# Performance work log

Measured on AMD Instinct MI355X. Metric: run time of the kernel, lower is better.

## Reference

```python
import jax, jax.numpy as jnp
import numpy as np

# Irreps config: 256x0e + 256x1e + 256x2e + 256x3e for both input and output.
MUL = 256
DIMS = (1, 3, 5, 7)          # (2l+1) for l = 0..3
OFFS = np.cumsum([0] + [MUL * d for d in DIMS]).tolist()  # [0,256,1024,2304,4096]
TOTAL_DIM = OFFS[-1]          # 4096
BATCH = 20000


def setup_inputs() -> dict:
    key = jax.random.key(0)
    ks = jax.random.split(key, 6)
    x = jax.random.normal(ks[0], (BATCH, TOTAL_DIM), dtype=jnp.float32)
    # per-path Linear weights, shape (mul_out, mul_in) like nn.Linear.weight,
    # kaiming_uniform_(a=sqrt(5)) => uniform(-1/sqrt(fan_in), 1/sqrt(fan_in))
    bound = 1.0 / np.sqrt(MUL)
    W = [jax.random.uniform(ks[i + 1], (MUL, MUL), dtype=jnp.float32,
                            minval=-bound, maxval=bound) for i in range(4)]
    bias = jnp.zeros((MUL,), dtype=jnp.float32)  # scalar (l=0) bias, init zeros
    return {"x": x, "W0": W[0], "W1": W[1], "W2": W[2], "W3": W[3], "bias": bias}


def reference(x, W0, W1, W2, W3, bias):
    Ws = (W0, W1, W2, W3)
    B = x.shape[0]
    out_chunks = []
    for l, (W, d) in enumerate(zip(Ws, DIMS)):
        # slice out this irrep block: (B, MUL*d) -> (B, MUL, d)
        xc = x[:, OFFS[l]:OFFS[l + 1]].reshape(B, MUL, d)
        # Linear over multiplicity channel: y[b,o,d] = sum_i W[o,i] * x[b,i,d]
        yc = jnp.einsum('oi,bid->bod', W, xc)
        out_chunks.append(yc.reshape(B, MUL * d))
    out = jnp.concatenate(out_chunks, axis=-1)  # (B, TOTAL_DIM)
    # bias on scalar (l=0) outputs only
    out = out.at[:, OFFS[0]:OFFS[1]].add(bias)
    return out
```

## Files before the change

### kernel.cpp

```cpp
#include <hip/hip_runtime.h>

#define BATCH_N 20000

typedef __attribute__((ext_vector_type(4))) float  f32x4;
typedef __attribute__((ext_vector_type(8))) __bf16 bf16x8;
typedef __attribute__((ext_vector_type(8))) short  s16x8;
typedef __attribute__((ext_vector_type(8))) unsigned short u16x8;
typedef __attribute__((ext_vector_type(4))) unsigned short u16x4;
typedef unsigned short u16;
typedef unsigned int   u32;

__device__ __forceinline__ u16 f2bf(float f) {
    union { float f; u32 u; } v; v.f = f;
    u32 r = v.u + 0x7fffu + ((v.u >> 16) & 1u);
    return (u16)(r >> 16);
}

template <typename C, typename V>
__device__ __forceinline__ auto mfma_bf16(V a, V b, C c, int)
    -> decltype(__builtin_amdgcn_mfma_f32_16x16x32_bf16(a, b, c, 0, 0, 0)) {
    return __builtin_amdgcn_mfma_f32_16x16x32_bf16(a, b, c, 0, 0, 0);
}
template <typename C, typename V>
__device__ __forceinline__ C mfma_bf16(V a, V b, C c, long) {
    return __builtin_amdgcn_mfma_f32_16x16x32_bf16(
        __builtin_bit_cast(s16x8, a), __builtin_bit_cast(s16x8, b), c, 0, 0, 0);
}

__device__ __forceinline__ bf16x8 cvt8(const float* p) {
    f32x4 v0 = *(const f32x4*)p;
    f32x4 v1 = *(const f32x4*)(p + 4);
    u16x8 raw = { f2bf(v0[0]), f2bf(v0[1]), f2bf(v0[2]), f2bf(v0[3]),
                  f2bf(v1[0]), f2bf(v1[1]), f2bf(v1[2]), f2bf(v1[3]) };
    return __builtin_bit_cast(bf16x8, raw);
}

template <typename WT>
__device__ __forceinline__ bf16x8 load_wfrag(const WT* p) {
    if constexpr (sizeof(WT) == 2) {
        return __builtin_bit_cast(bf16x8, *(const u16x8*)p);
    } else {
        return cvt8(p);
    }
}

template <typename WT>
__device__ __forceinline__ void run_l0(const float* __restrict__ x,
                                       const WT* __restrict__ W,
                                       const float* __restrict__ bias,
                                       float* __restrict__ out, int tile) {
    const int b0   = tile * 64;
    const int tid  = threadIdx.x;
    const int lane = tid & 63;
    const int wv   = tid >> 6;
    const int l15  = lane & 15;
    const int qd   = lane >> 4;

    f32x4 zero = {0.f, 0.f, 0.f, 0.f};
    f32x4 acc[4][4];
#pragma unroll
    for (int r = 0; r < 4; ++r)
#pragma unroll
        for (int c = 0; c < 4; ++c) acc[r][c] = zero;

    int brow[4];
#pragma unroll
    for (int r = 0; r < 4; ++r) {
        int b = b0 + r * 16 + l15;
        brow[r] = (b < BATCH_N) ? b : (BATCH_N - 1);
    }

#pragma unroll
    for (int kc = 0; kc < 4; ++kc) {
#pragma unroll
        for (int ks = 0; ks < 2; ++ks) {
            const int kg = kc * 64 + ks * 32 + qd * 8;
            bf16x8 a[4], bb[4];
#pragma unroll
            for (int r = 0; r < 4; ++r)
                a[r] = cvt8(x + (size_t)brow[r] * 4096 + kg);
#pragma unroll
            for (int c = 0; c < 4; ++c)
                bb[c] = load_wfrag(W + (size_t)(wv * 64 + c * 16 + l15) * 256 + kg);
#pragma unroll
            for (int r = 0; r < 4; ++r)
#pragma unroll
                for (int c = 0; c < 4; ++c)
                    acc[r][c] = mfma_bf16(a[r], bb[c], acc[r][c], 0);
        }
    }

    float bv[4];
#pragma unroll
    for (int c = 0; c < 4; ++c) bv[c] = bias[wv * 64 + c * 16 + l15];

#pragma unroll
    for (int r = 0; r < 4; ++r)
#pragma unroll
        for (int rg = 0; rg < 4; ++rg) {
            int b = b0 + r * 16 + qd * 4 + rg;
            if (b < BATCH_N) {
#pragma unroll
                for (int c = 0; c < 4; ++c)
                    out[(size_t)b * 4096 + wv * 64 + c * 16 + l15] = acc[r][c][rg] + bv[c];
            }
        }
}

template <int D, int NB, int OFF, typename WT>
__device__ __forceinline__ void run_gen(const float* __restrict__ x,
                                        const WT* __restrict__ W,
                                        float* __restrict__ out,
                                        u16* xs, int tile) {
    constexpr int CM = NB * D;
    const int b0   = tile * NB;
    const int nb   = (BATCH_N - b0 < NB) ? (BATCH_N - b0) : NB;
    const int cols = nb * D;
    const int tid  = threadIdx.x;
    const int lane = tid & 63;
    const int wv   = tid >> 6;
    const int l15  = lane & 15;
    const int qd   = lane >> 4;
    const int ob   = wv * 64;

    f32x4 zero = {0.f, 0.f, 0.f, 0.f};
    f32x4 acc[4][4];
#pragma unroll
    for (int r = 0; r < 4; ++r)
#pragma unroll
        for (int c = 0; c < 4; ++c) acc[r][c] = zero;

    for (int kc = 0; kc < 4; ++kc) {
#pragma unroll
        for (int g0 = 0; g0 < CM * 16; g0 += 256) {
            int g = g0 + tid;
            if (g < CM * 16) {
                int col = g % CM;
                int kq  = g / CM;
                if (col < cols) {
                    int bq = col / D;
                    int m  = col - bq * D;
                    const float* gp = x + (size_t)(b0 + bq) * 4096 + OFF +
                                      (kc * 64 + kq * 4) * D + m;
                    u16x4 u = { f2bf(gp[0]), f2bf(gp[D]), f2bf(gp[2 * D]), f2bf(gp[3 * D]) };
                    *(u16x4*)(xs + col * 72 + kq * 4) = u;
                }
            }
        }
        __syncthreads();

#pragma unroll
        for (int ks = 0; ks < 2; ++ks) {
            const int kg = kc * 64 + ks * 32 + qd * 8;
            const int kl = ks * 32 + qd * 8;
            bf16x8 a[4], bb[4];
#pragma unroll
            for (int r = 0; r < 4; ++r)
                a[r] = load_wfrag(W + (size_t)(ob + r * 16 + l15) * 256 + kg);
#pragma unroll
            for (int c = 0; c < 4; ++c)
                bb[c] = __builtin_bit_cast(bf16x8,
                            *(const u16x8*)(xs + (c * 16 + l15) * 72 + kl));
#pragma unroll
            for (int r = 0; r < 4; ++r)
#pragma unroll
                for (int c = 0; c < 4; ++c)
                    acc[r][c] = mfma_bf16(a[r], bb[c], acc[r][c], 0);
        }
        __syncthreads();
    }

#pragma unroll
    for (int c = 0; c < 4; ++c) {
        int col = c * 16 + l15;
        if (col < cols) {
            int bq = col / D;
            int m  = col - bq * D;
            float* op = out + (size_t)(b0 + bq) * 4096 + OFF + m;
#pragma unroll
            for (int r = 0; r < 4; ++r)
#pragma unroll
                for (int rg = 0; rg < 4; ++rg) {
                    int o = ob + r * 16 + qd * 4 + rg;
                    op[o * D] = acc[r][c][rg];
                }
        }
    }
}

template <typename WT>
__global__ __launch_bounds__(256) void so3_main(const float* __restrict__ x,
        const WT* __restrict__ W0, const WT* __restrict__ W1,
        const WT* __restrict__ W2, const WT* __restrict__ W3,
        const float* __restrict__ bias, float* __restrict__ out) {
    __shared__ __align__(16) u16 xs[64 * 72];
    int bid = blockIdx.x;
    if (bid < 313) {
        run_l0(x, W0, bias, out, bid);
    } else if (bid < 1266) {
        run_gen<3, 21, 256>(x, W1, out, xs, bid - 313);
    } else if (bid < 2933) {
        run_gen<5, 12, 1024>(x, W2, out, xs, bid - 1266);
    } else {
        run_gen<7, 9, 2304>(x, W3, out, xs, bid - 2933);
    }
}

__global__ __launch_bounds__(256) void w_to_bf16(const float* __restrict__ W0,
        const float* __restrict__ W1, const float* __restrict__ W2,
        const float* __restrict__ W3, u16* __restrict__ ws) {
    const float* Wt[4] = {W0, W1, W2, W3};
    const float* W = Wt[blockIdx.y];
    u16* o = ws + (size_t)blockIdx.y * 65536;
    int t = blockIdx.x * 256 + threadIdx.x;
    f32x4 v = ((const f32x4*)W)[t];
    u16x4 u = { f2bf(v[0]), f2bf(v[1]), f2bf(v[2]), f2bf(v[3]) };
    ((u16x4*)o)[t] = u;
}

extern "C" void kernel_launch(void* const* d_in, const int* in_sizes, int n_in,
                              void* d_out, int out_size, void* d_ws, size_t ws_size,
                              hipStream_t stream) {
    const float* x    = (const float*)d_in[0];
    const float* W0   = (const float*)d_in[1];
    const float* W1   = (const float*)d_in[2];
    const float* W2   = (const float*)d_in[3];
    const float* W3   = (const float*)d_in[4];
    const float* bias = (const float*)d_in[5];
    float* out = (float*)d_out;

    if (ws_size >= 4ull * 65536ull * sizeof(u16)) {
        u16* wsW = (u16*)d_ws;
        w_to_bf16<<<dim3(64, 4), 256, 0, stream>>>(W0, W1, W2, W3, wsW);
        so3_main<u16><<<5156, 256, 0, stream>>>(x, wsW, wsW + 65536,
                                                wsW + 2 * 65536, wsW + 3 * 65536,
                                                bias, out);
    } else {
        so3_main<float><<<5156, 256, 0, stream>>>(x, W0, W1, W2, W3, bias, out);
    }
}
```

Baseline: 725.5 us.

## Double-buffer x tiles in LDS with register prefetch across k-chunks

The l>0 path now stages x through registers. It loads and converts the next k-chunk from global memory while MFMAs run on the current LDS buffer, then writes it into a second LDS buffer. This drops one __syncthreads per iteration and hides global load latency behind compute. The cost is double the LDS footprint, extra staging registers, and a launch_bounds occupancy hint of 5 blocks per CU, which may force register spilling.

```diff
diff --git a/kernel.cpp b/kernel.cpp
--- a/kernel.cpp
+++ b/kernel.cpp
@@ -112,7 +112,10 @@
                                         const WT* __restrict__ W,
                                         float* __restrict__ out,
                                         u16* xs, int tile) {
-    constexpr int CM = NB * D;
+    constexpr int CM  = NB * D;
+    constexpr int NIT = CM * 16;
+    constexpr int SUB = (NIT + 255) / 256;
+    constexpr int BUF = 64 * 72;
     const int b0   = tile * NB;
     const int nb   = (BATCH_N - b0 < NB) ? (BATCH_N - b0) : NB;
     const int cols = nb * D;
@@ -130,24 +133,47 @@
 #pragma unroll
         for (int c = 0; c < 4; ++c) acc[r][c] = zero;
 
-    for (int kc = 0; kc < 4; ++kc) {
-#pragma unroll
-        for (int g0 = 0; g0 < CM * 16; g0 += 256) {
-            int g = g0 + tid;
-            if (g < CM * 16) {
-                int col = g % CM;
-                int kq  = g / CM;
+    u16x4 st[SUB];
+
+    auto gload = [&](int kc) {
+#pragma unroll
+        for (int s = 0; s < SUB; ++s) {
+            const int g = s * 256 + tid;
+            if (g < NIT) {
+                const int col = g % CM;
+                const int kq  = g / CM;
                 if (col < cols) {
-                    int bq = col / D;
-                    int m  = col - bq * D;
+                    const int bq = col / D;
+                    const int m  = col - bq * D;
                     const float* gp = x + (size_t)(b0 + bq) * 4096 + OFF +
                                       (kc * 64 + kq * 4) * D + m;
-                    u16x4 u = { f2bf(gp[0]), f2bf(gp[D]), f2bf(gp[2 * D]), f2bf(gp[3 * D]) };
-                    *(u16x4*)(xs + col * 72 + kq * 4) = u;
+                    st[s] = (u16x4){ f2bf(gp[0]), f2bf(gp[D]),
+                                     f2bf(gp[2 * D]), f2bf(gp[3 * D]) };
                 }
             }
         }
+    };
+    auto lwrite = [&](u16* buf) {
+#pragma unroll
+        for (int s = 0; s < SUB; ++s) {
+            const int g = s * 256 + tid;
+            if (g < NIT) {
+                const int col = g % CM;
+                const int kq  = g / CM;
+                if (col < cols)
+                    *(u16x4*)(buf + col * 72 + kq * 4) = st[s];
+            }
+        }
+    };
+
+    gload(0);
+    lwrite(xs);
+
+#pragma unroll
+    for (int kc = 0; kc < 4; ++kc) {
+        u16* cur = xs + (kc & 1) * BUF;
         __syncthreads();
+        if (kc < 3) gload(kc + 1);
 
 #pragma unroll
         for (int ks = 0; ks < 2; ++ks) {
@@ -160,14 +186,15 @@
 #pragma unroll
             for (int c = 0; c < 4; ++c)
                 bb[c] = __builtin_bit_cast(bf16x8,
-                            *(const u16x8*)(xs + (c * 16 + l15) * 72 + kl));
+                            *(const u16x8*)(cur + (c * 16 + l15) * 72 + kl));
 #pragma unroll
             for (int r = 0; r < 4; ++r)
 #pragma unroll
                 for (int c = 0; c < 4; ++c)
                     acc[r][c] = mfma_bf16(a[r], bb[c], acc[r][c], 0);
         }
-        __syncthreads();
+
+        if (kc < 3) lwrite(xs + ((kc + 1) & 1) * BUF);
     }
 
 #pragma unroll
@@ -189,11 +216,11 @@
 }
 
 template <typename WT>
-__global__ __launch_bounds__(256) void so3_main(const float* __restrict__ x,
+__global__ __launch_bounds__(256, 5) void so3_main(const float* __restrict__ x,
         const WT* __restrict__ W0, const WT* __restrict__ W1,
         const WT* __restrict__ W2, const WT* __restrict__ W3,
         const float* __restrict__ bias, float* __restrict__ out) {
-    __shared__ __align__(16) u16 xs[64 * 72];
+    __shared__ __align__(16) u16 xs[2 * 64 * 72];
     int bid = blockIdx.x;
     if (bid < 313) {
         run_l0(x, W0, bias, out, bid);
```

Measured after the change: 1.028 ms. 41.6% more time.

## Double-buffer LDS staging of x tiles with register prefetch in run_gen

Applied to the files above, without the earlier changes.

Converts the per-k-chunk global-to-LDS staging in the l>0 paths into a double-buffered software pipeline. The next chunk's global loads go into registers before the MFMAs and are written to the alternate LDS buffer afterwards, which removes one barrier per iteration and hides global load latency behind compute. Address computation is also hoisted out of the loop. This doubles LDS use per block and raises register pressure, which could lower occupancy.

```diff
diff --git a/kernel.cpp b/kernel.cpp
--- a/kernel.cpp
+++ b/kernel.cpp
@@ -112,7 +112,9 @@
                                         const WT* __restrict__ W,
                                         float* __restrict__ out,
                                         u16* xs, int tile) {
-    constexpr int CM = NB * D;
+    constexpr int CM  = NB * D;
+    constexpr int NIT = CM * 16;
+    constexpr int BUF = 64 * 72;
     const int b0   = tile * NB;
     const int nb   = (BATCH_N - b0 < NB) ? (BATCH_N - b0) : NB;
     const int cols = nb * D;
@@ -130,24 +132,43 @@
 #pragma unroll
         for (int c = 0; c < 4; ++c) acc[r][c] = zero;
 
+    const float* gp[4];
+    int          lo[4];
+    u16x4        st[4];
+#pragma unroll
+    for (int s = 0; s < 4; ++s) {
+        const int g   = s * 256 + tid;
+        const int col = g % CM;
+        const int kq  = g / CM;
+        const int bq  = col / D;
+        const int m   = col - bq * D;
+        const bool ok = (g < NIT) && (col < cols);
+        gp[s] = ok ? (x + (size_t)(b0 + bq) * 4096 + OFF + (kq * 4) * D + m)
+                   : x;
+        lo[s] = ok ? (col * 72 + kq * 4)
+                   : 64;
+    }
+
+#define GLOAD(kc_)                                                         \
+    _Pragma("unroll")                                                      \
+    for (int s = 0; s < 4; ++s) {                                          \
+        const float* p = gp[s] + (kc_) * 64 * D;                           \
+        st[s] = (u16x4){ f2bf(p[0]), f2bf(p[D]),                           \
+                         f2bf(p[2 * D]), f2bf(p[3 * D]) };                 \
+    }
+#define LWRITE(buf_)                                                       \
+    _Pragma("unroll")                                                      \
+    for (int s = 0; s < 4; ++s)                                            \
+        *(u16x4*)((buf_) + lo[s]) = st[s];
+
+    GLOAD(0);
+    LWRITE(xs);
+
+#pragma unroll
     for (int kc = 0; kc < 4; ++kc) {
-#pragma unroll
-        for (int g0 = 0; g0 < CM * 16; g0 += 256) {
-            int g = g0 + tid;
-            if (g < CM * 16) {
-                int col = g % CM;
-                int kq  = g / CM;
-                if (col < cols) {
-                    int bq = col / D;
-                    int m  = col - bq * D;
-                    const float* gp = x + (size_t)(b0 + bq) * 4096 + OFF +
-                                      (kc * 64 + kq * 4) * D + m;
-                    u16x4 u = { f2bf(gp[0]), f2bf(gp[D]), f2bf(gp[2 * D]), f2bf(gp[3 * D]) };
-                    *(u16x4*)(xs + col * 72 + kq * 4) = u;
-                }
-            }
-        }
+        u16* cur = xs + (kc & 1) * BUF;
         __syncthreads();
+        if (kc < 3) GLOAD(kc + 1);
 
 #pragma unroll
         for (int ks = 0; ks < 2; ++ks) {
@@ -160,15 +181,18 @@
 #pragma unroll
             for (int c = 0; c < 4; ++c)
                 bb[c] = __builtin_bit_cast(bf16x8,
-                            *(const u16x8*)(xs + (c * 16 + l15) * 72 + kl));
+                            *(const u16x8*)(cur + (c * 16 + l15) * 72 + kl));
 #pragma unroll
             for (int r = 0; r < 4; ++r)
 #pragma unroll
                 for (int c = 0; c < 4; ++c)
                     acc[r][c] = mfma_bf16(a[r], bb[c], acc[r][c], 0);
         }
-        __syncthreads();
-    }
+
+        if (kc < 3) LWRITE(xs + ((kc + 1) & 1) * BUF);
+    }
+#undef GLOAD
+#undef LWRITE
 
 #pragma unroll
     for (int c = 0; c < 4; ++c) {
@@ -193,7 +217,7 @@
         const WT* __restrict__ W0, const WT* __restrict__ W1,
         const WT* __restrict__ W2, const WT* __restrict__ W3,
         const float* __restrict__ bias, float* __restrict__ out) {
-    __shared__ __align__(16) u16 xs[64 * 72];
+    __shared__ __align__(16) u16 xs[2 * 64 * 72];
     int bid = blockIdx.x;
     if (bid < 313) {
         run_l0(x, W0, bias, out, bid);
```

Result: faster. 675.9 us (-6.8%).
